# Kernel tuning notes

Hardware: AMD Instinct MI355X
Metric: run time of the kernel (lower is better)

## Reference

```python
import jax, jax.numpy as jnp
import numpy as np

B, S = 16, 768
DCOG, DENV, NENV = 64, 32, 8
D, N, L, FF, NC = 512, 64, 6, 2048, 1
DIL = (1, 2, 4, 8)
EPS = 1e-5


def _layer_norm(x, g, b):
    m = x.mean(-1, keepdims=True)
    v = ((x - m) ** 2).mean(-1, keepdims=True)
    return (x - m) * jax.lax.rsqrt(v + EPS) * g + b


def _conv1d(x, w, b, d):
    # x: (B, D, S), w: (O, I, K); 'same' padding = (K-1)*d//2 = d for K=3
    y = jax.lax.conv_general_dilated(x, w, (1,), [(d, d)], rhs_dilation=(d,),
                                     dimension_numbers=('NCH', 'OIH', 'NCH'))
    return y + b[None, :, None]


def _combine(c1, c2):
    a1, b1 = c1
    a2, b2 = c2
    return a1 * a2, a2 * b1 + b2


def _forward(x_cog, cw1, cb1, cw2, cb2, env_emb, ew1, eb1, ew2, eb2,
             fw1, fb1, fw2, fb2, pos_enc, conv_w, conv_b, wm_w, wm_b,
             ssm_w, ssm_b, A_log, ffw1, ffb1, ffw2, ffb2,
             g1, be1, g2, be2, pw1, pb1, pw2, pb2, x_env):
    # Dual-channel feature processor (dropout = identity at eval)
    z = x_cog / jnp.maximum(jnp.linalg.norm(x_cog, axis=-1, keepdims=True), 1e-12)
    z = jnp.maximum(z @ cw1 + cb1, 0.0) @ cw2 + cb2
    e = env_emb[x_env].mean(-2)                      # (B,S,NENV,D) -> (B,S,D)
    e = jnp.maximum(e @ ew1 + eb1, 0.0) @ ew2 + eb2
    hf = jnp.concatenate([z, e], -1)
    hf = jnp.maximum(hf @ fw1 + fb1, 0.0) @ fw2 + fb2
    h = hf + pos_enc[:S][None]

    def layer_step(h, p):
        cw, cb, wmw, wmb, sw, sb, alog, w1, b1, w2, b2, g1_, be1_, g2_, be2_ = p
        # Multi-scale dilated conv
        xt = h.transpose(0, 2, 1)                    # (B, D, S)
        outs = [_conv1d(xt, cw[i], cb[i], DIL[i]) for i in range(4)]
        alpha = jax.nn.softmax(xt.mean(-1) @ wmw + wmb, -1)   # (B, 4)
        hm = sum(alpha[:, i, None, None] * outs[i] for i in range(4)).transpose(0, 2, 1)
        h1 = _layer_norm(hm + h, g1_, be1_)
        # Selective state-space (diagonal A), parallel associative scan
        proj = jnp.einsum('bsd,kdn->kbsn', h1, sw) + sb[:, None, None, :]
        delta, Bt, Ct = jax.nn.softplus(proj[0]), proj[1], proj[2]
        a = jnp.exp(alog[None, None, :] * delta)     # (B, S, N)
        bu = Bt * h1[..., :N]
        _, hs = jax.lax.associative_scan(_combine, (a, bu), axis=1)
        y = jnp.sum(Ct * hs, -1, keepdims=True)      # (B, S, 1)
        h2 = _layer_norm(y + h1, g2_, be2_)          # broadcast over D, as in torch
        return jnp.maximum(h2 @ w1 + b1, 0.0) @ w2 + b2 + h2, None

    h, _ = jax.lax.scan(layer_step, h, (conv_w, conv_b, wm_w, wm_b, ssm_w, ssm_b,
                                        A_log, ffw1, ffb1, ffw2, ffb2, g1, be1, g2, be2))
    hg = h.mean(1)                                   # adaptive avg pool over S
    return jnp.maximum(hg @ pw1 + pb1, 0.0) @ pw2 + pb2


def setup_inputs():
    ks = iter(jax.random.split(jax.random.key(0), 48))
    def rn(shape, s=0.02):
        return jax.random.normal(next(ks), shape, jnp.float32) * s
    return {
        'x_cog': rn((B, S, DCOG), 1.0),
        'cw1': rn((DCOG, D)), 'cb1': jnp.zeros(D), 'cw2': rn((D, D)), 'cb2': jnp.zeros(D),
        'env_emb': rn((DENV, D), 1.0),
        'ew1': rn((D, D)), 'eb1': jnp.zeros(D), 'ew2': rn((D, D)), 'eb2': jnp.zeros(D),
        'fw1': rn((2 * D, D)), 'fb1': jnp.zeros(D), 'fw2': rn((D, D)), 'fb2': jnp.zeros(D),
        'pos_enc': rn((1000, D), 1.0),
        'conv_w': rn((L, 4, D, D, 3)), 'conv_b': jnp.zeros((L, 4, D)),
        'wm_w': rn((L, D, 4)), 'wm_b': jnp.zeros((L, 4)),
        'ssm_w': rn((L, 3, D, N)), 'ssm_b': jnp.zeros((L, 3, N)),
        'A_log': -jnp.abs(rn((L, N), 1.0)),
        'ffw1': rn((L, D, FF)), 'ffb1': jnp.zeros((L, FF)),
        'ffw2': rn((L, FF, D)), 'ffb2': jnp.zeros((L, D)),
        'g1': jnp.ones((L, D)), 'be1': jnp.zeros((L, D)),
        'g2': jnp.ones((L, D)), 'be2': jnp.zeros((L, D)),
        'pw1': rn((D, D // 2)), 'pb1': jnp.zeros(D // 2),
        'pw2': rn((D // 2, NC)), 'pb2': jnp.zeros(NC),
        'x_env': jax.random.randint(next(ks), (B, S, NENV), 0, DENV, jnp.int32),
    }


def reference(x_cog, cw1, cb1, cw2, cb2, env_emb, ew1, eb1, ew2, eb2,
              fw1, fb1, fw2, fb2, pos_enc, conv_w, conv_b, wm_w, wm_b,
              ssm_w, ssm_b, A_log, ffw1, ffb1, ffw2, ffb2,
              g1, be1, g2, be2, pw1, pb1, pw2, pb2, x_env):
    return _forward(x_cog, cw1, cb1, cw2, cb2, env_emb, ew1, eb1, ew2, eb2,
                    fw1, fb1, fw2, fb2, pos_enc, conv_w, conv_b, wm_w, wm_b,
                    ssm_w, ssm_b, A_log, ffw1, ffb1, ffw2, ffb2,
                    g1, be1, g2, be2, pw1, pb1, pw2, pb2, x_env)
```

## Files before the change

### kernel.cpp

```cpp
#include <hip/hip_runtime.h>
#include <cstdint>
#include <cstddef>

namespace {

constexpr int B = 16, S = 768, BS = B * S, D = 512, FF = 2048, L = 6;
constexpr float EPS = 1e-5f;

typedef float f32x4 __attribute__((ext_vector_type(4)));
typedef _Float16 f16x8 __attribute__((ext_vector_type(8)));

__device__ __forceinline__ float wave_sum(float v) {
#pragma unroll
  for (int o = 32; o > 0; o >>= 1) v += __shfl_xor(v, o, 64);
  return v;
}

__device__ __forceinline__ short f16b(float x) {
  const _Float16 h = (_Float16)x;
  return __builtin_bit_cast(short, h);
}
__device__ __forceinline__ float h2f(short s) {
  return (float)__builtin_bit_cast(_Float16, s);
}

__device__ __forceinline__ void gload16(const void* g, void* l) {
  __builtin_amdgcn_global_load_lds(
      (const __attribute__((address_space(1))) void*)g,
      (__attribute__((address_space(3))) void*)l, 16, 0, 0);
}


template <bool RELU, bool RESID, bool FOUT, bool PACK>
__global__ __launch_bounds__(256, 3) void gemm_h(
    const short* __restrict__ A, int lda, const short* __restrict__ Wt,
    int ldw, int Klen, const float* __restrict__ bias,
    const float* __restrict__ resid, int ldr, int rmod,
    float* __restrict__ fout, int ldc, short* __restrict__ ph, int ldp) {
  __shared__ alignas(16) short sAh[8192], sBh[8192];
  const int tid = threadIdx.x;
  const unsigned Nt = gridDim.x;
  const unsigned lin = blockIdx.y * Nt + blockIdx.x;
  const unsigned cpx = (Nt * gridDim.y) >> 3;
  const unsigned swz = (lin & 7) * cpx + (lin >> 3);
  const int bn = (int)(swz % Nt) * 128, bm = (int)(swz / Nt) * 128;
  const int wave = tid >> 6, lane = tid & 63;
  const int wr = (wave >> 1) * 64, wc = (wave & 1) * 64;
  const int lr = lane & 15, sl = lane >> 4;
  const short* Ab = A + (size_t)bm * lda;
  const short* Wb = Wt + (size_t)bn * ldw;
  f32x4 acc[4][4] = {};
  for (int kk = 0; kk < Klen; kk += 64) {
#pragma unroll
    for (int jj = 0; jj < 4; ++jj) {
      const int G = jj * 256 + tid;
      const int srow = G >> 3, sl0 = G & 7;
      const int gsl = sl0 ^ (srow & 7);
      const int dst = G * 8;
      gload16(Ab + (size_t)srow * lda + kk + gsl * 8, &sAh[dst]);
      gload16(Wb + (size_t)srow * ldw + kk + gsl * 8, &sBh[dst]);
    }
    __syncthreads();
#pragma unroll
    for (int ks = 0; ks < 2; ++ks) {
      f16x8 aH[4], bH[4];
#pragma unroll
      for (int m = 0; m < 4; ++m) {
        const int r = wr + m * 16 + lr;
        aH[m] = *(const f16x8*)&sAh[r * 64 + (((ks * 4 + sl) ^ (r & 7)) * 8)];
      }
#pragma unroll
      for (int n = 0; n < 4; ++n) {
        const int r = wc + n * 16 + lr;
        bH[n] = *(const f16x8*)&sBh[r * 64 + (((ks * 4 + sl) ^ (r & 7)) * 8)];
      }
#pragma unroll
      for (int m = 0; m < 4; ++m)
#pragma unroll
        for (int n = 0; n < 4; ++n)
          acc[m][n] = __builtin_amdgcn_mfma_f32_16x16x32_f16(aH[m], bH[n],
                                                             acc[m][n], 0, 0, 0);
    }
    __syncthreads();
  }
  const int r4 = sl * 4;
#pragma unroll
  for (int m = 0; m < 4; ++m) {
#pragma unroll
    for (int r = 0; r < 4; ++r) {
      const int mm = bm + wr + m * 16 + r4 + r;
#pragma unroll
      for (int n = 0; n < 4; ++n) {
        const int col = bn + wc + n * 16 + lr;
        float v = acc[m][n][r] + bias[col];
        if (RELU) v = fmaxf(v, 0.f);
        if (RESID) {
          const int rr = rmod ? (mm % rmod) : mm;
          v += resid[(size_t)rr * ldr + col];
        }
        if (FOUT) fout[(size_t)mm * ldc + col] = v;
        if (PACK) ph[(size_t)mm * ldp + col] = f16b(v);
      }
    }
  }
}

template <bool RELU, bool RESID, bool FOUT, bool PACK, bool CSUM>
__global__ __launch_bounds__(256, 3) void gemm_h64(
    const short* __restrict__ A, int lda, const short* __restrict__ Wt,
    int ldw, int Klen, const float* __restrict__ bias,
    const float* __restrict__ resid, int ldr, int rmod,
    float* __restrict__ fout, int ldc, short* __restrict__ ph, int ldp,
    float* __restrict__ part) {
  __shared__ alignas(16) short sAh[8192], sBh[4096];
  __shared__ float csLds[2][64];
  const int tid = threadIdx.x;
  const unsigned Nt = gridDim.x;
  const unsigned lin = blockIdx.y * Nt + blockIdx.x;
  const unsigned cpx = (Nt * gridDim.y) >> 3;
  const unsigned swz = (lin & 7) * cpx + (lin >> 3);
  const int bn = (int)(swz % Nt) * 64, bmt = (int)(swz / Nt);
  const int bm = bmt * 128;
  const int wave = tid >> 6, lane = tid & 63;
  const int wr = (wave >> 1) * 64, wc = (wave & 1) * 32;
  const int lr = lane & 15, sl = lane >> 4;
  const short* Ab = A + (size_t)bm * lda;
  const short* Wb = Wt + (size_t)bn * ldw;
  f32x4 acc[4][2] = {};
  for (int kk = 0; kk < Klen; kk += 64) {
#pragma unroll
    for (int jj = 0; jj < 4; ++jj) {
      const int G = jj * 256 + tid;
      const int srow = G >> 3, sl0 = G & 7;
      const int gsl = sl0 ^ (srow & 7);
      gload16(Ab + (size_t)srow * lda + kk + gsl * 8, &sAh[G * 8]);
    }
#pragma unroll
    for (int jj = 0; jj < 2; ++jj) {
      const int G = jj * 256 + tid;
      const int srow = G >> 3, sl0 = G & 7;
      const int gsl = sl0 ^ (srow & 7);
      gload16(Wb + (size_t)srow * ldw + kk + gsl * 8, &sBh[G * 8]);
    }
    __syncthreads();
#pragma unroll
    for (int ks = 0; ks < 2; ++ks) {
      f16x8 aH[4], bH[2];
#pragma unroll
      for (int m = 0; m < 4; ++m) {
        const int r = wr + m * 16 + lr;
        aH[m] = *(const f16x8*)&sAh[r * 64 + (((ks * 4 + sl) ^ (r & 7)) * 8)];
      }
#pragma unroll
      for (int n = 0; n < 2; ++n) {
        const int r = wc + n * 16 + lr;
        bH[n] = *(const f16x8*)&sBh[r * 64 + (((ks * 4 + sl) ^ (r & 7)) * 8)];
      }
#pragma unroll
      for (int m = 0; m < 4; ++m)
#pragma unroll
        for (int n = 0; n < 2; ++n)
          acc[m][n] = __builtin_amdgcn_mfma_f32_16x16x32_f16(aH[m], bH[n],
                                                             acc[m][n], 0, 0, 0);
    }
    __syncthreads();
  }
  const int r4 = sl * 4;
  float cs[2] = {0.f, 0.f};
#pragma unroll
  for (int m = 0; m < 4; ++m) {
#pragma unroll
    for (int r = 0; r < 4; ++r) {
      const int mm = bm + wr + m * 16 + r4 + r;
#pragma unroll
      for (int n = 0; n < 2; ++n) {
        const int col = bn + wc + n * 16 + lr;
        float v = acc[m][n][r] + bias[col];
        if (RELU) v = fmaxf(v, 0.f);
        if (RESID) {
          const int rr = rmod ? (mm % rmod) : mm;
          v += resid[(size_t)rr * ldr + col];
        }
        if (FOUT) fout[(size_t)mm * ldc + col] = v;
        if (PACK) ph[(size_t)mm * ldp + col] = f16b(v);
        if (CSUM) cs[n] += v;
      }
    }
  }
  if constexpr (CSUM) {
#pragma unroll
    for (int n = 0; n < 2; ++n) {
      cs[n] += __shfl_xor(cs[n], 16, 64);
      cs[n] += __shfl_xor(cs[n], 32, 64);
    }
    if (sl == 0) {
      csLds[wave >> 1][wc + lr] = cs[0];
      csLds[wave >> 1][wc + 16 + lr] = cs[1];
    }
    __syncthreads();
    if (tid < 64)
      part[(size_t)bmt * 512 + bn + tid] = csLds[0][tid] + csLds[1][tid];
  }
}

__global__ __launch_bounds__(256, 3) void conv_zp_k(
    const short* __restrict__ hp, const short* __restrict__ wt8,
    const short* __restrict__ wmix, const float* __restrict__ alpha,
    const short* __restrict__ zpadS, short* __restrict__ P) {
  __shared__ alignas(16) short sAh[8192], sBh[8192];
  const int tid = threadIdx.x;
  const unsigned lin = blockIdx.x;
  const unsigned swz = (lin & 7) * 96 + (lin >> 3);
  const int zp = (int)(swz / 384);
  const unsigned rem = swz % 384;
  const int bn = (int)(rem & 3) * 128;
  const int bmt = (int)(rem >> 2);
  const int b = bmt / 6, s0 = (bmt % 6) * 128, gm0 = bmt * 128;
  const int wave = tid >> 6, lane = tid & 63;
  const int wr = (wave >> 1) * 64, wc = (wave & 1) * 64;
  const int lr = lane & 15, sl = lane >> 4;
  const short* hb = hp + (size_t)b * S * 512;
  f32x4 accF[4][4] = {};
#pragma unroll
  for (int zi = 0; zi < 2; ++zi) {
    const int z = zp * 2 + zi;
    const int dd = 1 << z;
    f32x4 acc[4][4] = {};
    for (int kk = 0; kk < 1024; kk += 64) {
      const int tap = kk >> 9;
      const int koff = kk & 511;
      const int off = tap ? dd : -dd;
#pragma unroll
      for (int jj = 0; jj < 4; ++jj) {
        const int G = jj * 256 + tid;
        const int srow = G >> 3, sl0 = G & 7;
        const int gsl = sl0 ^ (srow & 7);
        const int dst = G * 8;
        const int gs = s0 + srow + off;
        const bool inb = ((unsigned)gs < (unsigned)S);
        const short* aBase = hb + (size_t)gs * 512 + koff + gsl * 8;
        gload16(inb ? aBase : zpadS, &sAh[dst]);
        gload16(wt8 + ((size_t)((z * 2 + tap) * 512 + bn + srow)) * 512 +
                    koff + gsl * 8,
                &sBh[dst]);
      }
      __syncthreads();
#pragma unroll
      for (int ks = 0; ks < 2; ++ks) {
        f16x8 aH[4], bH[4];
#pragma unroll
        for (int m = 0; m < 4; ++m) {
          const int r = wr + m * 16 + lr;
          aH[m] =
              *(const f16x8*)&sAh[r * 64 + (((ks * 4 + sl) ^ (r & 7)) * 8)];
        }
#pragma unroll
        for (int n = 0; n < 4; ++n) {
          const int r = wc + n * 16 + lr;
          bH[n] =
              *(const f16x8*)&sBh[r * 64 + (((ks * 4 + sl) ^ (r & 7)) * 8)];
        }
#pragma unroll
        for (int m = 0; m < 4; ++m)
#pragma unroll
          for (int n = 0; n < 4; ++n)
            acc[m][n] = __builtin_amdgcn_mfma_f32_16x16x32_f16(
                aH[m], bH[n], acc[m][n], 0, 0, 0);
      }
      __syncthreads();
    }
    const float al = alpha[b * 4 + z];
#pragma unroll
    for (int m = 0; m < 4; ++m)
#pragma unroll
      for (int n = 0; n < 4; ++n)
#pragma unroll
        for (int r = 0; r < 4; ++r) accF[m][n][r] += al * acc[m][n][r];
  }
  const short* Wm = wmix + (size_t)b * 512 * 512;
  for (int kc = 0; kc < 256; kc += 64) {
    const int koff = zp * 256 + kc;
#pragma unroll
    for (int jj = 0; jj < 4; ++jj) {
      const int G = jj * 256 + tid;
      const int srow = G >> 3, sl0 = G & 7;
      const int gsl = sl0 ^ (srow & 7);
      const int dst = G * 8;
      gload16(hb + (size_t)(s0 + srow) * 512 + koff + gsl * 8, &sAh[dst]);
      gload16(Wm + (size_t)(bn + srow) * 512 + koff + gsl * 8, &sBh[dst]);
    }
    __syncthreads();
#pragma unroll
    for (int ks = 0; ks < 2; ++ks) {
      f16x8 aH[4], bH[4];
#pragma unroll
      for (int m = 0; m < 4; ++m) {
        const int r = wr + m * 16 + lr;
        aH[m] = *(const f16x8*)&sAh[r * 64 + (((ks * 4 + sl) ^ (r & 7)) * 8)];
      }
#pragma unroll
      for (int n = 0; n < 4; ++n) {
        const int r = wc + n * 16 + lr;
        bH[n] = *(const f16x8*)&sBh[r * 64 + (((ks * 4 + sl) ^ (r & 7)) * 8)];
      }
#pragma unroll
      for (int m = 0; m < 4; ++m)
#pragma unroll
        for (int n = 0; n < 4; ++n)
          accF[m][n] = __builtin_amdgcn_mfma_f32_16x16x32_f16(
              aH[m], bH[n], accF[m][n], 0, 0, 0);
    }
    __syncthreads();
  }
  short* Pz = P + (size_t)zp * ((size_t)BS * D);
  const int r4 = sl * 4;
#pragma unroll
  for (int m = 0; m < 4; ++m)
#pragma unroll
    for (int r = 0; r < 4; ++r) {
      const int mm = gm0 + wr + m * 16 + r4 + r;
#pragma unroll
      for (int n = 0; n < 4; ++n)
        Pz[(size_t)mm * D + bn + wc + n * 16 + lr] = f16b(accF[m][n][r]);
    }
}

__global__ __launch_bounds__(256) void ln3_k(
    const short* __restrict__ P0, const short* __restrict__ P1,
    const float* __restrict__ resid, const float* __restrict__ cbmix,
    const float* __restrict__ g1, const float* __restrict__ b1,
    const float* __restrict__ g2, const float* __restrict__ b2,
    float* __restrict__ fout, short* __restrict__ pout) {
  const int row = blockIdx.x * 4 + (threadIdx.x >> 6);
  const int lane = threadIdx.x & 63;
  const int bb = row / S;
  const size_t base = (size_t)row * D;
  float v[8];
  float s = 0.f;
#pragma unroll
  for (int j = 0; j < 8; ++j) {
    const int c = lane + 64 * j;
    v[j] = h2f(P0[base + c]) + h2f(P1[base + c]) + resid[base + c] +
           cbmix[(size_t)bb * D + c];
    s += v[j];
  }
  s = wave_sum(s);
  const float m1 = s * (1.f / D);
  float q = 0.f;
#pragma unroll
  for (int j = 0; j < 8; ++j) { const float d = v[j] - m1; q += d * d; }
  q = wave_sum(q);
  const float r1 = rsqrtf(q * (1.f / D) + EPS);
  float y[8];
  float s2 = 0.f;
#pragma unroll
  for (int j = 0; j < 8; ++j) {
    const int c = lane + 64 * j;
    y[j] = (v[j] - m1) * r1 * g1[c] + b1[c];
    s2 += y[j];
  }
  s2 = wave_sum(s2);
  const float m2 = s2 * (1.f / D);
  float q2 = 0.f;
#pragma unroll
  for (int j = 0; j < 8; ++j) { const float d = y[j] - m2; q2 += d * d; }
  q2 = wave_sum(q2);
  const float r2 = rsqrtf(q2 * (1.f / D) + EPS);
  float* frow = fout + base;
  short* prow = pout + (size_t)row * 512;
#pragma unroll
  for (int j = 0; j < 8; ++j) {
    const int c = lane + 64 * j;
    const float o = (y[j] - m2) * r2 * g2[c] + b2[c];
    frow[c] = o;
    prow[c] = f16b(o);
  }
}

__global__ __launch_bounds__(256) void pack_wt_k(const float* __restrict__ W,
                                                 short* __restrict__ out,
                                                 int K, int N) {
  __shared__ short t[64][68];
  const int n0 = blockIdx.x * 64, k0 = blockIdx.y * 64;
  const int ln = threadIdx.x & 63, w4 = threadIdx.x >> 6;
#pragma unroll
  for (int it = 0; it < 16; ++it) {
    const int kr = it * 4 + w4;
    t[kr][ln] = f16b(W[(size_t)(k0 + kr) * N + n0 + ln]);
  }
  __syncthreads();
#pragma unroll
  for (int it = 0; it < 16; ++it) {
    const int nr = it * 4 + w4;
    out[(size_t)(n0 + nr) * K + k0 + ln] = t[ln][nr];
  }
}

__global__ __launch_bounds__(256) void convprep_k(
    const float* __restrict__ cw, const float* __restrict__ alpha,
    short* __restrict__ out8, short* __restrict__ wm) {
  const int bid = blockIdx.x;
  if (bid < 8192) {
    const int idx = bid * 256 + threadIdx.x;
    const int c = idx & 511, o = (idx >> 9) & 511, seg = idx >> 18;
    const int z = seg >> 1, t = (seg & 1) * 2;
    out8[((size_t)seg * D + o) * D + c] =
        f16b(cw[(((size_t)z * D + o) * D + c) * 3 + t]);
  } else {
    __shared__ float sal[64];
    if (threadIdx.x < 64) sal[threadIdx.x] = alpha[threadIdx.x];
    __syncthreads();
    const int idx = (bid - 8192) * 256 + threadIdx.x;
    const int c = idx & 511, o = idx >> 9;
    float w[4];
#pragma unroll
    for (int z = 0; z < 4; ++z)
      w[z] = cw[(((size_t)z * D + o) * D + c) * 3 + 1];
#pragma unroll
    for (int b = 0; b < 16; ++b) {
      const float v = sal[b * 4 + 0] * w[0] + sal[b * 4 + 1] * w[1] +
                      sal[b * 4 + 2] * w[2] + sal[b * 4 + 3] * w[3];
      wm[((size_t)b * D + o) * D + c] = f16b(v);
    }
  }
}

__global__ __launch_bounds__(256) void zero_k(float* __restrict__ p) {
  p[threadIdx.x] = 0.f;
  p[threadIdx.x + 256] = 0.f;
}

__global__ __launch_bounds__(64) void alpha_k(const float* __restrict__ part,
                                              const float* __restrict__ wmw,
                                              const float* __restrict__ wmb,
                                              const float* __restrict__ cb,
                                              float* __restrict__ alpha,
                                              float* __restrict__ cbmix) {
  const int b = blockIdx.x, t = threadIdx.x;
  float p0 = 0, p1 = 0, p2 = 0, p3 = 0;
  for (int d = t; d < D; d += 64) {
    float xm = 0;
#pragma unroll
    for (int c = 0; c < 6; ++c) xm += part[((size_t)(b * 6 + c)) * D + d];
    xm *= (1.f / S);
    p0 += xm * wmw[d * 4 + 0];
    p1 += xm * wmw[d * 4 + 1];
    p2 += xm * wmw[d * 4 + 2];
    p3 += xm * wmw[d * 4 + 3];
  }
  p0 = wave_sum(p0); p1 = wave_sum(p1);
  p2 = wave_sum(p2); p3 = wave_sum(p3);
  const float l0 = p0 + wmb[0], l1 = p1 + wmb[1];
  const float l2 = p2 + wmb[2], l3 = p3 + wmb[3];
  const float mx = fmaxf(fmaxf(l0, l1), fmaxf(l2, l3));
  const float e0 = expf(l0 - mx), e1 = expf(l1 - mx);
  const float e2 = expf(l2 - mx), e3 = expf(l3 - mx);
  const float inv = 1.f / (e0 + e1 + e2 + e3);
  const float a0 = e0 * inv, a1 = e1 * inv, a2 = e2 * inv, a3 = e3 * inv;
  if (t == 0) {
    alpha[b * 4 + 0] = a0;
    alpha[b * 4 + 1] = a1;
    alpha[b * 4 + 2] = a2;
    alpha[b * 4 + 3] = a3;
  }
  for (int c = t; c < D; c += 64)
    cbmix[(size_t)b * D + c] =
        a0 * cb[c] + a1 * cb[D + c] + a2 * cb[2 * D + c] + a3 * cb[3 * D + c];
}

__global__ __launch_bounds__(256) void embed_k(const int* __restrict__ xe,
                                               const float* __restrict__ emb,
                                               short* __restrict__ out) {
  const int r = blockIdx.x;
  int idx[8];
#pragma unroll
  for (int j = 0; j < 8; ++j) idx[j] = xe[r * 8 + j];
  short* o = out + (size_t)r * 512;
  for (int d = threadIdx.x; d < D; d += 256) {
    float s = 0.f;
#pragma unroll
    for (int j = 0; j < 8; ++j) s += emb[(size_t)idx[j] * D + d];
    o[d] = f16b(s * 0.125f);
  }
}

__global__ __launch_bounds__(256) void norml2_k(const float* __restrict__ x,
                                                short* __restrict__ out) {
  const int r = blockIdx.x * 4 + (threadIdx.x >> 6);
  const int lane = threadIdx.x & 63;
  const float v = x[(size_t)r * 64 + lane];
  const float s = wave_sum(v * v);
  const float nrm = fmaxf(sqrtf(s), 1e-12f);
  out[(size_t)r * 64 + lane] = f16b(v / nrm);
}

__global__ __launch_bounds__(256) void head_k(
    const float* __restrict__ part, const float* __restrict__ pw1,
    const float* __restrict__ pb1, const float* __restrict__ pw2,
    const float* __restrict__ pb2, float* __restrict__ out) {
  __shared__ float hg[D];
  __shared__ float red[256];
  const int b = blockIdx.x, t = threadIdx.x;
  for (int d = t; d < D; d += 256) {
    float s = 0.f;
#pragma unroll
    for (int c = 0; c < 6; ++c) s += part[((size_t)(b * 6 + c)) * D + d];
    hg[d] = s * (1.f / S);
  }
  __syncthreads();
  float s = pb1[t];
  for (int d = 0; d < D; ++d) s = fmaf(hg[d], pw1[(size_t)d * 256 + t], s);
  s = fmaxf(s, 0.f);
  red[t] = s * pw2[t];
  __syncthreads();
  for (int o = 128; o > 0; o >>= 1) {
    if (t < o) red[t] += red[t + o];
    __syncthreads();
  }
  if (t == 0) out[b] = red[0] + pb2[0];
}

}

extern "C" void kernel_launch(void* const* d_in, const int* in_sizes, int n_in,
                              void* d_out, int out_size, void* d_ws,
                              size_t ws_size, hipStream_t stream) {
  const float* x_cog = (const float*)d_in[0];
  const float* cw1 = (const float*)d_in[1];
  const float* cb1 = (const float*)d_in[2];
  const float* cw2 = (const float*)d_in[3];
  const float* cb2 = (const float*)d_in[4];
  const float* env_emb = (const float*)d_in[5];
  const float* ew1 = (const float*)d_in[6];
  const float* eb1 = (const float*)d_in[7];
  const float* ew2 = (const float*)d_in[8];
  const float* eb2 = (const float*)d_in[9];
  const float* fw1 = (const float*)d_in[10];
  const float* fb1 = (const float*)d_in[11];
  const float* fw2 = (const float*)d_in[12];
  const float* fb2 = (const float*)d_in[13];
  const float* pos_enc = (const float*)d_in[14];
  const float* conv_w = (const float*)d_in[15];
  const float* conv_b = (const float*)d_in[16];
  const float* wm_w = (const float*)d_in[17];
  const float* wm_b = (const float*)d_in[18];
  const float* ffw1 = (const float*)d_in[22];
  const float* ffb1 = (const float*)d_in[23];
  const float* ffw2 = (const float*)d_in[24];
  const float* ffb2 = (const float*)d_in[25];
  const float* g1 = (const float*)d_in[26];
  const float* be1 = (const float*)d_in[27];
  const float* g2 = (const float*)d_in[28];
  const float* be2 = (const float*)d_in[29];
  const float* pw1 = (const float*)d_in[30];
  const float* pb1 = (const float*)d_in[31];
  const float* pw2 = (const float*)d_in[32];
  const float* pb2 = (const float*)d_in[33];
  const int* x_env = (const int*)d_in[34];
  float* out = (float*)d_out;

  float* ws = (float*)d_ws;
  float* Hbuf = ws;
  float* TBuf = Hbuf + 6291456;
  float* PART2 = TBuf + 6291456;
  float* ALPHAB = PART2 + 65536;
  float* ZPADF = ALPHAB + 64;
  float* CBMIX = ZPADF + 512;
  short* R = (short*)(CBMIX + 8192);
  short* WCONV8 = R;
  short* WFFP = R + 2097152;
  short* WMIX = R + 3145728;
  short* convPh = R + 7340032;
  short* APFF = R + 7340032;
  short* HPACK = R + 32505856;
  short* CONC = R;
  short* PK1 = R + 25165824;
  short* PK2 = R + 25165824 + 6291456;
  short* WPBF = WFFP;

  const dim3 blk(256);
  const dim3 gS(8, 96, 1);
  const dim3 gF(16, 96, 1);

  zero_k<<<1, blk, 0, stream>>>(ZPADF);

  norml2_k<<<BS / 4, blk, 0, stream>>>(x_cog, PK1);
  pack_wt_k<<<dim3(8, 1), blk, 0, stream>>>(cw1, WPBF, 64, 512);
  gemm_h64<true, false, false, true, false><<<gS, blk, 0, stream>>>(
      PK1, 64, WPBF, 64, 64, cb1, nullptr, 0, 0, nullptr, 0, PK2, 512,
      nullptr);
  pack_wt_k<<<dim3(8, 8), blk, 0, stream>>>(cw2, WPBF, 512, 512);
  gemm_h64<false, false, false, true, false><<<gS, blk, 0, stream>>>(
      PK2, 512, WPBF, 512, 512, cb2, nullptr, 0, 0, nullptr, 0, CONC, 2048,
      nullptr);
  embed_k<<<BS, blk, 0, stream>>>(x_env, env_emb, PK1);
  pack_wt_k<<<dim3(8, 8), blk, 0, stream>>>(ew1, WPBF, 512, 512);
  gemm_h64<true, false, false, true, false><<<gS, blk, 0, stream>>>(
      PK1, 512, WPBF, 512, 512, eb1, nullptr, 0, 0, nullptr, 0, PK2, 512,
      nullptr);
  pack_wt_k<<<dim3(8, 8), blk, 0, stream>>>(ew2, WPBF, 512, 512);
  gemm_h64<false, false, false, true, false><<<gS, blk, 0, stream>>>(
      PK2, 512, WPBF, 512, 512, eb2, nullptr, 0, 0, nullptr, 0, CONC + 512,
      2048, nullptr);
  pack_wt_k<<<dim3(8, 16), blk, 0, stream>>>(fw1, WPBF, 1024, 512);
  gemm_h64<true, false, false, true, false><<<gS, blk, 0, stream>>>(
      CONC, 2048, WPBF, 1024, 1024, fb1, nullptr, 0, 0, nullptr, 0, PK1, 512,
      nullptr);
  pack_wt_k<<<dim3(8, 8), blk, 0, stream>>>(fw2, WPBF, 512, 512);
  gemm_h64<false, true, true, true, true><<<gS, blk, 0, stream>>>(
      PK1, 512, WPBF, 512, 512, fb2, pos_enc, 512, S, Hbuf, 512, HPACK, 512,
      PART2);

  for (int l = 0; l < L; ++l) {
    const float* cwl = conv_w + (size_t)l * 4 * D * D * 3;
    alpha_k<<<B, dim3(64), 0, stream>>>(PART2, wm_w + (size_t)l * D * 4,
                                        wm_b + l * 4,
                                        conv_b + (size_t)l * 4 * D, ALPHAB,
                                        CBMIX);
    convprep_k<<<9216, blk, 0, stream>>>(cwl, ALPHAB, WCONV8, WMIX);
    conv_zp_k<<<768, blk, 0, stream>>>(HPACK, WCONV8, WMIX, ALPHAB,
                                       (const short*)ZPADF, convPh);
    ln3_k<<<BS / 4, blk, 0, stream>>>(convPh, convPh + (size_t)BS * D, Hbuf,
                                      CBMIX, g1 + l * D, be1 + l * D,
                                      g2 + l * D, be2 + l * D, TBuf, HPACK);
    pack_wt_k<<<dim3(32, 8), blk, 0, stream>>>(ffw1 + (size_t)l * D * FF,
                                               WFFP, 512, 2048);
    gemm_h<true, false, false, true><<<gF, blk, 0, stream>>>(
        HPACK, 512, WFFP, 512, 512, ffb1 + (size_t)l * FF, nullptr, 0, 0,
        nullptr, 0, APFF, 2048);
    pack_wt_k<<<dim3(8, 32), blk, 0, stream>>>(ffw2 + (size_t)l * FF * D,
                                               WFFP, 2048, 512);
    gemm_h64<false, true, true, true, true><<<gS, blk, 0, stream>>>(
        APFF, 2048, WFFP, 2048, 2048, ffb2 + (size_t)l * D, TBuf, 512, 0,
        Hbuf, 512, HPACK, 512, PART2);
  }

  head_k<<<B, blk, 0, stream>>>(PART2, pw1, pb1, pw2, pb2, out);
}
```

Measured before the change: 1.212 ms.

## Drop fp32 residual stream, carry hidden state only in packed fp16

Removes the fp32 hidden-state buffers (Hbuf/TBuf). Layer norm and FFN residual adds now read the fp16 packed activation instead of fp32 copies, and the fp32 writes from the GEMM epilogues and ln3 are gone. This cuts global memory traffic per layer and frees workspace. The cost is extra rounding in the residual path, and the FFN2 GEMM now reads and writes HPACK in place as both residual and output.

```diff
diff --git a/kernel.cpp b/kernel.cpp
--- a/kernel.cpp
+++ b/kernel.cpp
@@ -31,12 +31,11 @@
 }
 
 
-template <bool RELU, bool RESID, bool FOUT, bool PACK>
+template <bool RELU, bool PACK>
 __global__ __launch_bounds__(256, 3) void gemm_h(
     const short* __restrict__ A, int lda, const short* __restrict__ Wt,
     int ldw, int Klen, const float* __restrict__ bias,
-    const float* __restrict__ resid, int ldr, int rmod,
-    float* __restrict__ fout, int ldc, short* __restrict__ ph, int ldp) {
+    short* __restrict__ ph, int ldp) {
   __shared__ alignas(16) short sAh[8192], sBh[8192];
   const int tid = threadIdx.x;
   const unsigned Nt = gridDim.x;
@@ -94,23 +93,18 @@
         const int col = bn + wc + n * 16 + lr;
         float v = acc[m][n][r] + bias[col];
         if (RELU) v = fmaxf(v, 0.f);
-        if (RESID) {
-          const int rr = rmod ? (mm % rmod) : mm;
-          v += resid[(size_t)rr * ldr + col];
-        }
-        if (FOUT) fout[(size_t)mm * ldc + col] = v;
         if (PACK) ph[(size_t)mm * ldp + col] = f16b(v);
       }
     }
   }
 }
 
-template <bool RELU, bool RESID, bool FOUT, bool PACK, bool CSUM>
+template <bool RELU, int RESM, bool PACK, bool CSUM>
 __global__ __launch_bounds__(256, 3) void gemm_h64(
     const short* __restrict__ A, int lda, const short* __restrict__ Wt,
     int ldw, int Klen, const float* __restrict__ bias,
-    const float* __restrict__ resid, int ldr, int rmod,
-    float* __restrict__ fout, int ldc, short* __restrict__ ph, int ldp,
+    const float* __restrict__ resid, const short* __restrict__ residS,
+    int ldr, int rmod, short* __restrict__ ph, int ldp,
     float* __restrict__ part) {
   __shared__ alignas(16) short sAh[8192], sBh[4096];
   __shared__ float csLds[2][64];
@@ -177,11 +171,11 @@
         const int col = bn + wc + n * 16 + lr;
         float v = acc[m][n][r] + bias[col];
         if (RELU) v = fmaxf(v, 0.f);
-        if (RESID) {
+        if (RESM == 1) {
           const int rr = rmod ? (mm % rmod) : mm;
           v += resid[(size_t)rr * ldr + col];
         }
-        if (FOUT) fout[(size_t)mm * ldc + col] = v;
+        if (RESM == 2) v += h2f(residS[(size_t)mm * ldr + col]);
         if (PACK) ph[(size_t)mm * ldp + col] = f16b(v);
         if (CSUM) cs[n] += v;
       }
@@ -327,10 +321,10 @@
 
 __global__ __launch_bounds__(256) void ln3_k(
     const short* __restrict__ P0, const short* __restrict__ P1,
-    const float* __restrict__ resid, const float* __restrict__ cbmix,
+    const short* __restrict__ hpk, const float* __restrict__ cbmix,
     const float* __restrict__ g1, const float* __restrict__ b1,
     const float* __restrict__ g2, const float* __restrict__ b2,
-    float* __restrict__ fout, short* __restrict__ pout) {
+    short* __restrict__ pout) {
   const int row = blockIdx.x * 4 + (threadIdx.x >> 6);
   const int lane = threadIdx.x & 63;
   const int bb = row / S;
@@ -340,7 +334,7 @@
 #pragma unroll
   for (int j = 0; j < 8; ++j) {
     const int c = lane + 64 * j;
-    v[j] = h2f(P0[base + c]) + h2f(P1[base + c]) + resid[base + c] +
+    v[j] = h2f(P0[base + c]) + h2f(P1[base + c]) + h2f(hpk[base + c]) +
            cbmix[(size_t)bb * D + c];
     s += v[j];
   }
@@ -366,14 +360,11 @@
   for (int j = 0; j < 8; ++j) { const float d = y[j] - m2; q2 += d * d; }
   q2 = wave_sum(q2);
   const float r2 = rsqrtf(q2 * (1.f / D) + EPS);
-  float* frow = fout + base;
-  short* prow = pout + (size_t)row * 512;
+  short* prow = pout + base;
 #pragma unroll
   for (int j = 0; j < 8; ++j) {
     const int c = lane + 64 * j;
-    const float o = (y[j] - m2) * r2 * g2[c] + b2[c];
-    frow[c] = o;
-    prow[c] = f16b(o);
+    prow[c] = f16b((y[j] - m2) * r2 * g2[c] + b2[c]);
   }
 }
 
@@ -560,9 +551,7 @@
   float* out = (float*)d_out;
 
   float* ws = (float*)d_ws;
-  float* Hbuf = ws;
-  float* TBuf = Hbuf + 6291456;
-  float* PART2 = TBuf + 6291456;
+  float* PART2 = ws;
   float* ALPHAB = PART2 + 65536;
   float* ZPADF = ALPHAB + 64;
   float* CBMIX = ZPADF + 512;
@@ -575,8 +564,8 @@
   short* HPACK = R + 32505856;
   short* CONC = R;
   short* PK1 = R + 25165824;
-  short* PK2 = R + 25165824 + 6291456;
-  short* WPBF = WFFP;
+  short* PK2 = R + 31457280;
+  short* WPBF = R + 38797312;
 
   const dim3 blk(256);
   const dim3 gS(8, 96, 1);
@@ -586,29 +575,28 @@
 
   norml2_k<<<BS / 4, blk, 0, stream>>>(x_cog, PK1);
   pack_wt_k<<<dim3(8, 1), blk, 0, stream>>>(cw1, WPBF, 64, 512);
-  gemm_h64<true, false, false, true, false><<<gS, blk, 0, stream>>>(
-      PK1, 64, WPBF, 64, 64, cb1, nullptr, 0, 0, nullptr, 0, PK2, 512,
-      nullptr);
+  gemm_h64<true, 0, true, false><<<gS, blk, 0, stream>>>(
+      PK1, 64, WPBF, 64, 64, cb1, nullptr, nullptr, 0, 0, PK2, 512, nullptr);
   pack_wt_k<<<dim3(8, 8), blk, 0, stream>>>(cw2, WPBF, 512, 512);
-  gemm_h64<false, false, false, true, false><<<gS, blk, 0, stream>>>(
-      PK2, 512, WPBF, 512, 512, cb2, nullptr, 0, 0, nullptr, 0, CONC, 2048,
+  gemm_h64<false, 0, true, false><<<gS, blk, 0, stream>>>(
+      PK2, 512, WPBF, 512, 512, cb2, nullptr, nullptr, 0, 0, CONC, 2048,
       nullptr);
   embed_k<<<BS, blk, 0, stream>>>(x_env, env_emb, PK1);
   pack_wt_k<<<dim3(8, 8), blk, 0, stream>>>(ew1, WPBF, 512, 512);
-  gemm_h64<true, false, false, true, false><<<gS, blk, 0, stream>>>(
-      PK1, 512, WPBF, 512, 512, eb1, nullptr, 0, 0, nullptr, 0, PK2, 512,
+  gemm_h64<true, 0, true, false><<<gS, blk, 0, stream>>>(
+      PK1, 512, WPBF, 512, 512, eb1, nullptr, nullptr, 0, 0, PK2, 512,
       nullptr);
   pack_wt_k<<<dim3(8, 8), blk, 0, stream>>>(ew2, WPBF, 512, 512);
-  gemm_h64<false, false, false, true, false><<<gS, blk, 0, stream>>>(
-      PK2, 512, WPBF, 512, 512, eb2, nullptr, 0, 0, nullptr, 0, CONC + 512,
-      2048, nullptr);
+  gemm_h64<false, 0, true, false><<<gS, blk, 0, stream>>>(
+      PK2, 512, WPBF, 512, 512, eb2, nullptr, nullptr, 0, 0, CONC + 512, 2048,
+      nullptr);
   pack_wt_k<<<dim3(8, 16), blk, 0, stream>>>(fw1, WPBF, 1024, 512);
-  gemm_h64<true, false, false, true, false><<<gS, blk, 0, stream>>>(
-      CONC, 2048, WPBF, 1024, 1024, fb1, nullptr, 0, 0, nullptr, 0, PK1, 512,
+  gemm_h64<true, 0, true, false><<<gS, blk, 0, stream>>>(
+      CONC, 2048, WPBF, 1024, 1024, fb1, nullptr, nullptr, 0, 0, PK1, 512,
       nullptr);
   pack_wt_k<<<dim3(8, 8), blk, 0, stream>>>(fw2, WPBF, 512, 512);
-  gemm_h64<false, true, true, true, true><<<gS, blk, 0, stream>>>(
-      PK1, 512, WPBF, 512, 512, fb2, pos_enc, 512, S, Hbuf, 512, HPACK, 512,
+  gemm_h64<false, 1, true, true><<<gS, blk, 0, stream>>>(
+      PK1, 512, WPBF, 512, 512, fb2, pos_enc, nullptr, 512, S, HPACK, 512,
       PART2);
 
   for (int l = 0; l < L; ++l) {
@@ -620,19 +608,19 @@
     convprep_k<<<9216, blk, 0, stream>>>(cwl, ALPHAB, WCONV8, WMIX);
     conv_zp_k<<<768, blk, 0, stream>>>(HPACK, WCONV8, WMIX, ALPHAB,
                                        (const short*)ZPADF, convPh);
-    ln3_k<<<BS / 4, blk, 0, stream>>>(convPh, convPh + (size_t)BS * D, Hbuf,
+    ln3_k<<<BS / 4, blk, 0, stream>>>(convPh, convPh + (size_t)BS * D, HPACK,
                                       CBMIX, g1 + l * D, be1 + l * D,
-                                      g2 + l * D, be2 + l * D, TBuf, HPACK);
+                                      g2 + l * D, be2 + l * D, HPACK);
     pack_wt_k<<<dim3(32, 8), blk, 0, stream>>>(ffw1 + (size_t)l * D * FF,
                                                WFFP, 512, 2048);
-    gemm_h<true, false, false, true><<<gF, blk, 0, stream>>>(
-        HPACK, 512, WFFP, 512, 512, ffb1 + (size_t)l * FF, nullptr, 0, 0,
-        nullptr, 0, APFF, 2048);
+    gemm_h<true, true><<<gF, blk, 0, stream>>>(HPACK, 512, WFFP, 512, 512,
+                                               ffb1 + (size_t)l * FF, APFF,
+                                               2048);
     pack_wt_k<<<dim3(8, 32), blk, 0, stream>>>(ffw2 + (size_t)l * FF * D,
                                                WFFP, 2048, 512);
-    gemm_h64<false, true, true, true, true><<<gS, blk, 0, stream>>>(
-        APFF, 2048, WFFP, 2048, 2048, ffb2 + (size_t)l * D, TBuf, 512, 0,
-        Hbuf, 512, HPACK, 512, PART2);
+    gemm_h64<false, 2, true, true><<<gS, blk, 0, stream>>>(
+        APFF, 2048, WFFP, 2048, 2048, ffb2 + (size_t)l * D, nullptr, HPACK,
+        512, 0, HPACK, 512, PART2);
   }
 
   head_k<<<B, blk, 0, stream>>>(PART2, pw1, pb1, pw2, pb2, out);
```

New measurement: 1.129 ms. 1.07x faster.
